# Kernel optimization log

Measured on AMD Instinct MI355X. Metric: run time of the kernel, lower is better.

The kernel has to match this reference:

```python
import jax, jax.numpy as jnp
import numpy as np

IN, HID, LAT, NLAYERS = 512, 256, 128, 2
B, T = 64, 512


def _init_params():
    key = jax.random.key(1)
    ks = jax.random.split(key, 24)

    def g(k, shape):
        fan_in = shape[-1]
        return (jax.random.normal(k, shape, jnp.float32) / np.sqrt(fan_in)).astype(jnp.float32)

    z = lambda n: jnp.zeros((n,), jnp.float32)
    return {
        # input projection
        'Wp': g(ks[0], (HID, IN)), 'bp': z(HID),
        # GRU layer 0 (input = hidden+latent = 384)
        'Wih0': g(ks[1], (3 * HID, HID + LAT)), 'Whh0': g(ks[2], (3 * HID, HID)),
        'bih0': z(3 * HID), 'bhh0': z(3 * HID),
        # GRU layer 1 (input = hidden)
        'Wih1': g(ks[3], (3 * HID, HID)), 'Whh1': g(ks[4], (3 * HID, HID)),
        'bih1': z(3 * HID), 'bhh1': z(3 * HID),
        # prior net
        'Wpr1': g(ks[5], (HID, HID)), 'bpr1': z(HID),
        'Wpr2': g(ks[6], (2 * LAT, HID)), 'bpr2': z(2 * LAT),
        # posterior net
        'Wpo1': g(ks[7], (HID, 2 * HID)), 'bpo1': z(HID),
        'Wpo2': g(ks[8], (2 * LAT, HID)), 'bpo2': z(2 * LAT),
        # decoder
        'Wd1': g(ks[9], (HID, HID + LAT)), 'bd1': z(HID),
        'Wd2': g(ks[10], (2 * IN, HID)), 'bd2': z(2 * IN),
    }


def setup_inputs() -> dict:
    key = jax.random.key(0)
    inp = {
        'x_seq': jax.random.normal(key, (B, T, IN), jnp.float32),
        'hidden': jnp.zeros((NLAYERS, B, HID), jnp.float32),
    }
    inp.update(_init_params())
    return inp


def _gelu(x):
    return jax.nn.gelu(x, approximate=False)  # torch default GELU is exact (erf)


def _gru_cell(x, h, Wih, Whh, bih, bhh):
    gi = x @ Wih.T + bih
    gh = h @ Whh.T + bhh
    ir, iz, inn = jnp.split(gi, 3, axis=-1)
    hr, hz, hn = jnp.split(gh, 3, axis=-1)
    r = jax.nn.sigmoid(ir + hr)
    zg = jax.nn.sigmoid(iz + hz)
    n = jnp.tanh(inn + r * hn)
    return (1.0 - zg) * n + zg * h


def _forward(x_seq, hidden, Wp, bp, Wih0, Whh0, bih0, bhh0, Wih1, Whh1, bih1, bhh1,
             Wpr1, bpr1, Wpr2, bpr2, Wpo1, bpo1, Wpo2, bpo2, Wd1, bd1, Wd2, bd2):
    x_proj = x_seq @ Wp.T + bp          # (B,T,HID)
    xs = jnp.swapaxes(x_proj, 0, 1)     # (T,B,HID)

    def step(h_carry, xt):
        h_prev = h_carry[-1]
        # prior p(z_t | h_{t-1})
        pp = _gelu(h_prev @ Wpr1.T + bpr1) @ Wpr2.T + bpr2
        p_mu, p_lv = jnp.split(pp, 2, axis=-1)
        # posterior q(z_t | h_{t-1}, x_t)
        qp = _gelu(jnp.concatenate([h_prev, xt], -1) @ Wpo1.T + bpo1) @ Wpo2.T + bpo2
        q_mu, q_lv = jnp.split(qp, 2, axis=-1)
        z_t = q_mu  # eval mode: use posterior mean
        # KL(q||p) diagonal Gaussians
        kl = 0.5 * (p_lv - q_lv + (jnp.exp(q_lv) + (q_mu - p_mu) ** 2) / jnp.exp(p_lv) - 1.0)
        kl = kl.sum(-1).mean()
        # 2-layer GRU single step
        gin = jnp.concatenate([xt, z_t], -1)
        h0 = _gru_cell(gin, h_carry[0], Wih0, Whh0, bih0, bhh0)
        h1 = _gru_cell(h0, h_carry[1], Wih1, Whh1, bih1, bhh1)
        h_new = jnp.stack([h0, h1], 0)
        # decode
        op = _gelu(jnp.concatenate([h1, z_t], -1) @ Wd1.T + bd1) @ Wd2.T + bd2
        o_mu, o_lv = jnp.split(op, 2, axis=-1)
        return h_new, (o_mu, o_lv, kl)

    hidden_f, (mus, lvs, kls) = jax.lax.scan(step, hidden, xs)
    pred_mu = jnp.swapaxes(mus, 0, 1)   # (B,T,IN)
    pred_lv = jnp.swapaxes(lvs, 0, 1)
    return pred_mu, pred_lv, kls.mean(), hidden_f


def reference(x_seq, hidden, Wp, bp, Wih0, Whh0, bih0, bhh0, Wih1, Whh1, bih1, bhh1,
              Wpr1, bpr1, Wpr2, bpr2, Wpo1, bpo1, Wpo2, bpo2, Wd1, bd1, Wd2, bd2):
    return _forward(x_seq, hidden, Wp, bp, Wih0, Whh0, bih0, bhh0, Wih1, Whh1, bih1, bhh1,
                    Wpr1, bpr1, Wpr2, bpr2, Wpo1, bpo1, Wpo2, bpo2, Wd1, bd1, Wd2, bd2)
```

## Files before the change

### kernel.cpp

```cpp
#include <hip/hip_runtime.h>
#include <math.h>

#define T_STEPS 512
#define NB      64
#define HID     256
#define IN_DIM  512
#define NWG     16

typedef __attribute__((ext_vector_type(8))) short bh8;
typedef __attribute__((ext_vector_type(4))) float f32x4;

#define SWZ(row, k, Kw) ((row)*(Kw) + ((k) ^ (((row)&7)*8)))

__device__ __forceinline__ float bf2f(unsigned short u) {
  union { unsigned u; float f; } v; v.u = ((unsigned)u) << 16; return v.f;
}
__device__ __forceinline__ unsigned short f2bf(float f) {
  union { float f; unsigned u; } v; v.f = f;
  unsigned r = v.u + 0x7FFFu + ((v.u >> 16) & 1u);
  return (unsigned short)(r >> 16);
}
__device__ __forceinline__ float geluf(float x) {
  return 0.5f * x * (1.f + erff(x * 0.70710678118654752f));
}
__device__ __forceinline__ float sigmf_(float x) { return 1.f / (1.f + __expf(-x)); }

__device__ __forceinline__ f32x4 mfma16(bh8 a, bh8 b, f32x4 c) {
  return __builtin_amdgcn_mfma_f32_16x16x32_bf16(a, b, c, 0, 0, 0);
}

__device__ __forceinline__ bh8 ldsh(const unsigned short* p) {
  bh8 r;
  asm volatile("global_load_dwordx4 %0, %1, off sc0 sc1" : "=v"(r) : "v"(p));
  return r;
}
__device__ __forceinline__ void stsh(unsigned short* p, unsigned short v) {
  unsigned v32 = v;
  asm volatile("global_store_short %0, %1, off sc0 sc1" :: "v"(p), "v"(v32) : "memory");
}
__device__ __forceinline__ void waitv0() {
  asm volatile("s_waitcnt vmcnt(0)" ::: "memory");
  __builtin_amdgcn_sched_barrier(0);
}

struct PrepArgs {
  const float *hidden;
  const float *Wp, *Wpo1, *Whh0, *Whh1, *Wih1, *Wih0, *Wpo2, *Wpr1, *Wpr2, *Wd1, *Wd2;
  unsigned short *Wp_b, *Wpo1cat, *Whh0_b, *Whh1_b, *Wih1_b, *WBcat, *Wpo2_b, *Wpr1_b, *Wpr2_b, *Wd1cat, *Wd2_b;
  unsigned short *H1_0, *h0b;
  unsigned *flags;
};

__global__ void prep1(PrepArgs a) {
  const int task = blockIdx.y;
  const int stride = gridDim.x * blockDim.x;
  const int i0 = blockIdx.x * blockDim.x + threadIdx.x;
  switch (task) {
    case 0:  for (int i=i0;i<131072;i+=stride) a.Wp_b[i]   = f2bf(a.Wp[i]);   break;
    case 1:  for (int i=i0;i<131072;i+=stride) a.Wpo1cat[i]= f2bf(a.Wpo1[i]); break;
    case 2:  for (int i=i0;i<196608;i+=stride) a.Whh0_b[i] = f2bf(a.Whh0[i]); break;
    case 3:  for (int i=i0;i<196608;i+=stride) a.Whh1_b[i] = f2bf(a.Whh1[i]); break;
    case 4:  for (int i=i0;i<196608;i+=stride) a.Wih1_b[i] = f2bf(a.Wih1[i]); break;
    case 5:  for (int i=i0;i<196608;i+=stride) { int c=i>>8, k=i&255;
               a.WBcat[c*512+k] = f2bf(a.Wih0[c*384+k]); } break;
    case 6:  for (int i=i0;i<65536;i+=stride)  a.Wpo2_b[i] = f2bf(a.Wpo2[i]); break;
    case 7:  for (int i=i0;i<65536;i+=stride)  a.Wpr1_b[i] = f2bf(a.Wpr1[i]); break;
    case 8:  for (int i=i0;i<65536;i+=stride)  a.Wpr2_b[i] = f2bf(a.Wpr2[i]); break;
    case 9:  for (int i=i0;i<98304;i+=stride)  a.Wd1cat[i] = f2bf(a.Wd1[i]);  break;
    case 10: for (int i=i0;i<262144;i+=stride) a.Wd2_b[i]  = f2bf(a.Wd2[i]);  break;
    case 11: for (int i=i0;i<16384;i+=stride)  a.H1_0[i] = f2bf(a.hidden[16384+i]); break;
    case 12: for (int i=i0;i<16384;i+=stride)  a.h0b[i]  = f2bf(a.hidden[i]);       break;
    case 15: for (int i=i0;i<1024;i+=stride)   a.flags[i] = 0u;                     break;
    default: break;
  }
}

__global__ void prep2(const float* __restrict__ Wih0, const float* __restrict__ Wpo2,
                      const float* __restrict__ bih0, const float* __restrict__ bpo2,
                      unsigned short* __restrict__ WBcat, float* __restrict__ bk0) {
  const int c = blockIdx.x;
  const int k = threadIdx.x;
  const float* wrow = Wih0 + c*384 + 256;
  float acc = 0.f;
  for (int j = 0; j < 128; ++j) acc += wrow[j] * Wpo2[j*256 + k];
  WBcat[c*512 + 256 + k] = f2bf(acc);
  if (k == 0) {
    float b = bih0[c];
    for (int j = 0; j < 128; ++j) b += wrow[j] * bpo2[j];
    bk0[c] = b;
  }
}

template<int EPI, bool A1F, bool A2F>
__global__ __launch_bounds__(256, 2) void gemm_k(
    const void* __restrict__ A1_, int lda1, int K1,
    const void* __restrict__ A2_, int lda2, int K2,
    const unsigned short* __restrict__ W, const float* __restrict__ bias,
    void* __restrict__ out_, int M, int N)
{
  __shared__ unsigned short sA[64*64];
  __shared__ unsigned short sW[64*64];
  const int m0 = blockIdx.x * 64, n0 = blockIdx.y * 64;
  const int tid = threadIdx.x, lane = tid & 63, wave = tid >> 6;
  const int Ktot = K1 + K2;
  f32x4 zero = {0.f,0.f,0.f,0.f};
  f32x4 acc[4] = {zero, zero, zero, zero};

  for (int kc = 0; kc < Ktot; kc += 64) {
    __syncthreads();
    #pragma unroll
    for (int i = 0; i < 2; ++i) {
      int cidx = tid*2 + i;
      int r = cidx >> 3, ko = (cidx & 7) * 8;
      int kg = kc + ko;
      alignas(16) unsigned short tmp[8];
      if (kg < K1) {
        if (A1F) {
          const float* p = (const float*)A1_ + (size_t)(m0 + r)*lda1 + kg;
          #pragma unroll
          for (int j = 0; j < 8; ++j) tmp[j] = f2bf(p[j]);
        } else {
          const unsigned short* p = (const unsigned short*)A1_ + (size_t)(m0 + r)*lda1 + kg;
          *(bh8*)tmp = *(const bh8*)p;
        }
      } else {
        int k2 = kg - K1;
        if (A2F) {
          const float* p = (const float*)A2_ + (size_t)(m0 + r)*lda2 + k2;
          #pragma unroll
          for (int j = 0; j < 8; ++j) tmp[j] = f2bf(p[j]);
        } else {
          const unsigned short* p = (const unsigned short*)A2_ + (size_t)(m0 + r)*lda2 + k2;
          *(bh8*)tmp = *(const bh8*)p;
        }
      }
      *(bh8*)&sA[SWZ(r, ko, 64)] = *(bh8*)tmp;
    }
    #pragma unroll
    for (int i = 0; i < 2; ++i) {
      int cidx = tid*2 + i;
      int r = cidx >> 3, ko = (cidx & 7) * 8;
      const unsigned short* p = W + (size_t)(n0 + r)*Ktot + kc + ko;
      *(bh8*)&sW[SWZ(r, ko, 64)] = *(const bh8*)p;
    }
    __syncthreads();
    #pragma unroll
    for (int ks = 0; ks < 2; ++ks) {
      int k0 = ks*32 + ((lane >> 4) << 3);
      int ar = 16*wave + (lane & 15);
      bh8 a = *(const bh8*)&sA[SWZ(ar, k0, 64)];
      #pragma unroll
      for (int nt = 0; nt < 4; ++nt) {
        int wr = nt*16 + (lane & 15);
        bh8 b = *(const bh8*)&sW[SWZ(wr, k0, 64)];
        acc[nt] = mfma16(a, b, acc[nt]);
      }
    }
  }
  #pragma unroll
  for (int nt = 0; nt < 4; ++nt) {
    int col = n0 + nt*16 + (lane & 15);
    float bv = bias[col];
    #pragma unroll
    for (int r = 0; r < 4; ++r) {
      int row = m0 + 16*wave + ((lane >> 4) << 2) + r;
      float v = acc[nt][r] + bv;
      if constexpr (EPI == 0) {
        ((float*)out_)[(size_t)row*N + col] = v;
      } else if constexpr (EPI == 1) {
        ((unsigned short*)out_)[(size_t)row*N + col] = f2bf(v);
      } else if constexpr (EPI == 2) {
        int b = row >> 9, t = row & 511;
        ((unsigned short*)out_)[((size_t)t*64 + b)*N + col] = f2bf(v);
      } else if constexpr (EPI == 3) {
        ((unsigned short*)out_)[(size_t)row*N + col] = f2bf(geluf(v));
      } else {
        int t = row >> 6, b = row & 63;
        float* o = (float*)out_;
        if (col < 512) o[(size_t)b*262144 + (size_t)t*512 + col] = v;
        else o[16777216 + (size_t)b*262144 + (size_t)t*512 + (col - 512)] = v;
      }
    }
  }
}

__device__ __forceinline__ void wbar_arrive(unsigned* flags, int g, int w, int lane, unsigned epoch) {
  asm volatile("s_waitcnt vmcnt(0)" ::: "memory");
  if (lane == 0) {
    unsigned* fp = flags + (g*4 + w)*16;
    asm volatile("global_store_dword %0, %1, off sc0 sc1" :: "v"(fp), "v"(epoch) : "memory");
  }
}
__device__ __forceinline__ void wbar_wait(unsigned* flags, int w, int lane, unsigned epoch) {
  if (lane < NWG) {
    const unsigned* fp = flags + (lane*4 + w)*16;
    unsigned v;
    do {
      asm volatile("global_load_dword %0, %1, off sc0 sc1\n\ts_waitcnt vmcnt(0)"
                   : "=v"(v) : "v"(fp) : "memory");
    } while (v < epoch);
  }
  __builtin_amdgcn_sched_barrier(0);
}

#define SEQ_LDS_BYTES ((16*512 + 48*256 + 48*256 + 48*512 + 48*256) * 2)

__global__ __launch_bounds__(256, 1) void seq_kernel(
    const unsigned short* __restrict__ gWQ,
    const unsigned short* __restrict__ gWH0,
    const unsigned short* __restrict__ gWH1,
    const unsigned short* __restrict__ gWB,
    const unsigned short* __restrict__ gWI1,
    const float* __restrict__ bpo1, const float* __restrict__ bhh0,
    const float* __restrict__ bhh1, const float* __restrict__ bih1,
    const float* __restrict__ bk0,
    const float* __restrict__ hidden0,
    const unsigned short* __restrict__ Xp,
    unsigned short* __restrict__ QP1,
    unsigned short* __restrict__ H1,
    unsigned short* __restrict__ h0b,
    unsigned* __restrict__ flags,
    float* __restrict__ outHid)
{
  extern __shared__ unsigned short lds[];
  unsigned short* WQ  = lds;
  unsigned short* WH0 = WQ  + 16*512;
  unsigned short* WH1 = WH0 + 48*256;
  unsigned short* WB  = WH1 + 48*256;
  unsigned short* WI1 = WB  + 48*512;
  const int g = blockIdx.x;
  const int tid = threadIdx.x;
  const int wave = tid >> 6, lane = tid & 63;

  for (int i = tid; i < 16*64; i += 256) { int p = i >> 6, ci = (i & 63) * 8;
    *(bh8*)&WQ[SWZ(p, ci, 512)] = *(const bh8*)&gWQ[(size_t)(16*g + p)*512 + ci]; }
  for (int i = tid; i < 48*32; i += 256) { int p = i >> 5, ci = (i & 31) * 8;
    int c = ((p >> 4) << 8) + 16*g + (p & 15);
    *(bh8*)&WH0[SWZ(p, ci, 256)] = *(const bh8*)&gWH0[(size_t)c*256 + ci]; }
  for (int i = tid; i < 48*32; i += 256) { int p = i >> 5, ci = (i & 31) * 8;
    int c = ((p >> 4) << 8) + 16*g + (p & 15);
    *(bh8*)&WH1[SWZ(p, ci, 256)] = *(const bh8*)&gWH1[(size_t)c*256 + ci]; }
  for (int i = tid; i < 48*64; i += 256) { int p = i >> 6, ci = (i & 63) * 8;
    int c = ((p >> 4) << 8) + 16*g + (p & 15);
    *(bh8*)&WB[SWZ(p, ci, 512)] = *(const bh8*)&gWB[(size_t)c*512 + ci]; }
  for (int i = tid; i < 48*32; i += 256) { int p = i >> 5, ci = (i & 31) * 8;
    int c = ((p >> 4) << 8) + 16*g + (p & 15);
    *(bh8*)&WI1[SWZ(p, ci, 256)] = *(const bh8*)&gWI1[(size_t)c*256 + ci]; }
  __syncthreads();

  const int col   = 16*g + (lane & 15);
  const int arow  = 16*wave + (lane & 15);
  const int crow0 = 16*wave + ((lane >> 4) << 2);
  const int koff  = ((lane >> 4) << 3);
  const float bq = bpo1[col];
  float bh0v[3], bh1v[3], bi1v[3], bk0v[3];
  #pragma unroll
  for (int e = 0; e < 3; ++e) {
    bh0v[e] = bhh0[e*256 + col]; bh1v[e] = bhh1[e*256 + col];
    bi1v[e] = bih1[e*256 + col]; bk0v[e] = bk0[e*256 + col];
  }
  float h0s[4], h1s[4];
  #pragma unroll
  for (int r = 0; r < 4; ++r) {
    h0s[r] = hidden0[(size_t)(crow0 + r)*HID + col];
    h1s[r] = hidden0[16384 + (size_t)(crow0 + r)*HID + col];
  }
  const f32x4 zero = {0.f,0.f,0.f,0.f};
  unsigned epoch = 0;

  f32x4 gh0a[3] = {zero, zero, zero};
  {
    bh8 h0i[8];
    #pragma unroll
    for (int j = 0; j < 8; ++j) h0i[j] = ldsh(h0b + (size_t)arow*HID + j*32 + koff);
    waitv0();
    #pragma unroll
    for (int ks = 0; ks < 8; ++ks) {
      int k0 = ks*32 + koff;
      #pragma unroll
      for (int e = 0; e < 3; ++e)
        gh0a[e] = mfma16(h0i[ks], *(const bh8*)&WH0[SWZ(e*16 + (lane&15), k0, 256)], gh0a[e]);
    }
  }
  bh8 xpr[8];
  #pragma unroll
  for (int j = 0; j < 8; ++j) xpr[j] = *(const bh8*)(Xp + (size_t)arow*HID + j*32 + koff);

  #pragma unroll 1
  for (int t = 0; t < T_STEPS; ++t) {
    const unsigned short* h1b = H1 + (size_t)t * (NB*HID);
    unsigned short* qp1t = QP1 + (size_t)t * (NB*HID);

    bh8 h1r[8];
    #pragma unroll
    for (int j = 0; j < 8; ++j) h1r[j] = ldsh(h1b + (size_t)arow*HID + j*32 + koff);
    waitv0();
    f32x4 aQ0 = zero, aQ1 = zero;
    #pragma unroll
    for (int ks = 0; ks < 8; ++ks) {
      int k0 = ks*32 + koff;
      aQ0 = mfma16(h1r[ks], *(const bh8*)&WQ[SWZ(lane & 15, k0, 512)], aQ0);
      aQ1 = mfma16(xpr[ks], *(const bh8*)&WQ[SWZ(lane & 15, 256 + k0, 512)], aQ1);
    }
    f32x4 gh1a[3] = {zero, zero, zero};
    #pragma unroll
    for (int ks = 0; ks < 8; ++ks) {
      int k0 = ks*32 + koff;
      #pragma unroll
      for (int e = 0; e < 3; ++e)
        gh1a[e] = mfma16(h1r[ks], *(const bh8*)&WH1[SWZ(e*16 + (lane&15), k0, 256)], gh1a[e]);
    }
    #pragma unroll
    for (int r = 0; r < 4; ++r) {
      float v = geluf(aQ0[r] + aQ1[r] + bq);
      stsh(qp1t + (size_t)(crow0 + r)*HID + col, f2bf(v));
    }
    ++epoch;
    wbar_arrive(flags, g, wave, lane, epoch);
    f32x4 gi[3] = {zero, zero, zero};
    #pragma unroll
    for (int ks = 0; ks < 8; ++ks) {
      int k0 = ks*32 + koff;
      #pragma unroll
      for (int e = 0; e < 3; ++e)
        gi[e] = mfma16(xpr[ks], *(const bh8*)&WB[SWZ(e*16 + (lane&15), k0, 512)], gi[e]);
    }
    wbar_wait(flags, wave, lane, epoch);

    bh8 qpr[8];
    #pragma unroll
    for (int j = 0; j < 8; ++j) qpr[j] = ldsh(qp1t + (size_t)arow*HID + j*32 + koff);
    waitv0();
    #pragma unroll
    for (int ks = 0; ks < 8; ++ks) {
      int k0 = ks*32 + koff;
      #pragma unroll
      for (int e = 0; e < 3; ++e)
        gi[e] = mfma16(qpr[ks], *(const bh8*)&WB[SWZ(e*16 + (lane&15), 256 + k0, 512)], gi[e]);
    }
    #pragma unroll
    for (int r = 0; r < 4; ++r) {
      float rr = sigmf_(gi[0][r] + bk0v[0] + gh0a[0][r] + bh0v[0]);
      float zz = sigmf_(gi[1][r] + bk0v[1] + gh0a[1][r] + bh0v[1]);
      float nn = tanhf(gi[2][r] + bk0v[2] + rr*(gh0a[2][r] + bh0v[2]));
      float hn = (1.f - zz)*nn + zz*h0s[r];
      h0s[r] = hn;
      stsh(h0b + (size_t)(crow0 + r)*HID + col, f2bf(hn));
    }
    ++epoch;
    wbar_arrive(flags, g, wave, lane, epoch);
    if (t + 1 < T_STEPS) {
      const unsigned short* xq = Xp + (size_t)(t + 1) * (NB*HID);
      #pragma unroll
      for (int j = 0; j < 8; ++j) xpr[j] = *(const bh8*)(xq + (size_t)arow*HID + j*32 + koff);
    }
    wbar_wait(flags, wave, lane, epoch);

    bh8 h0n[8];
    #pragma unroll
    for (int j = 0; j < 8; ++j) h0n[j] = ldsh(h0b + (size_t)arow*HID + j*32 + koff);
    waitv0();
    f32x4 gi1[3] = {zero, zero, zero};
    #pragma unroll
    for (int ks = 0; ks < 8; ++ks) {
      int k0 = ks*32 + koff;
      #pragma unroll
      for (int e = 0; e < 3; ++e)
        gi1[e] = mfma16(h0n[ks], *(const bh8*)&WI1[SWZ(e*16 + (lane&15), k0, 256)], gi1[e]);
    }
    unsigned short* h1n = H1 + (size_t)(t + 1) * (NB*HID);
    #pragma unroll
    for (int r = 0; r < 4; ++r) {
      float rr = sigmf_(gi1[0][r] + bi1v[0] + gh1a[0][r] + bh1v[0]);
      float zz = sigmf_(gi1[1][r] + bi1v[1] + gh1a[1][r] + bh1v[1]);
      float nn = tanhf(gi1[2][r] + bi1v[2] + rr*(gh1a[2][r] + bh1v[2]));
      float hv = (1.f - zz)*nn + zz*h1s[r];
      h1s[r] = hv;
      stsh(h1n + (size_t)(crow0 + r)*HID + col, f2bf(hv));
    }
    ++epoch;
    wbar_arrive(flags, g, wave, lane, epoch);
    if (t + 1 < T_STEPS) {
      gh0a[0] = zero; gh0a[1] = zero; gh0a[2] = zero;
      #pragma unroll
      for (int ks = 0; ks < 8; ++ks) {
        int k0 = ks*32 + koff;
        #pragma unroll
        for (int e = 0; e < 3; ++e)
          gh0a[e] = mfma16(h0n[ks], *(const bh8*)&WH0[SWZ(e*16 + (lane&15), k0, 256)], gh0a[e]);
      }
    }
    wbar_wait(flags, wave, lane, epoch);
  }

  #pragma unroll
  for (int r = 0; r < 4; ++r) {
    int row = crow0 + r;
    outHid[(size_t)row*HID + col]         = h0s[r];
    outHid[16384 + (size_t)row*HID + col] = h1s[r];
  }
}

__global__ void kl1(const float* __restrict__ Q, const unsigned short* __restrict__ Ppb,
                    float* __restrict__ part) {
  const int m0 = blockIdx.x * 64;
  float s = 0.f;
  for (int i = threadIdx.x; i < 64*128; i += 256) {
    int m = m0 + (i >> 7), j = i & 127;
    float qm = Q[(size_t)m*256 + j],        ql = Q[(size_t)m*256 + 128 + j];
    float pm = bf2f(Ppb[(size_t)m*256 + j]), pl = bf2f(Ppb[(size_t)m*256 + 128 + j]);
    float d = qm - pm;
    s += 0.5f * (pl - ql + (expf(ql) + d*d) * expf(-pl) - 1.f);
  }
  for (int o = 32; o > 0; o >>= 1) s += __shfl_down(s, o);
  __shared__ float red[4];
  if ((threadIdx.x & 63) == 0) red[threadIdx.x >> 6] = s;
  __syncthreads();
  if (threadIdx.x == 0) part[blockIdx.x] = red[0] + red[1] + red[2] + red[3];
}
__global__ void kl2(const float* __restrict__ part, float* __restrict__ out) {
  float s = 0.f;
  for (int i = threadIdx.x; i < 512; i += 256) s += part[i];
  for (int o = 32; o > 0; o >>= 1) s += __shfl_down(s, o);
  __shared__ float red[4];
  if ((threadIdx.x & 63) == 0) red[threadIdx.x >> 6] = s;
  __syncthreads();
  if (threadIdx.x == 0) out[0] = (red[0] + red[1] + red[2] + red[3]) / 32768.f;
}

extern "C" void kernel_launch(void* const* d_in, const int* in_sizes, int n_in,
                              void* d_out, int out_size, void* d_ws, size_t ws_size,
                              hipStream_t stream) {
  const float* x_seq  = (const float*)d_in[0];
  const float* hidden = (const float*)d_in[1];
  const float* Wp   = (const float*)d_in[2];  const float* bp   = (const float*)d_in[3];
  const float* Wih0 = (const float*)d_in[4];  const float* Whh0 = (const float*)d_in[5];
  const float* bih0 = (const float*)d_in[6];  const float* bhh0 = (const float*)d_in[7];
  const float* Wih1 = (const float*)d_in[8];  const float* Whh1 = (const float*)d_in[9];
  const float* bih1 = (const float*)d_in[10]; const float* bhh1 = (const float*)d_in[11];
  const float* Wpr1 = (const float*)d_in[12]; const float* bpr1 = (const float*)d_in[13];
  const float* Wpr2 = (const float*)d_in[14]; const float* bpr2 = (const float*)d_in[15];
  const float* Wpo1 = (const float*)d_in[16]; const float* bpo1 = (const float*)d_in[17];
  const float* Wpo2 = (const float*)d_in[18]; const float* bpo2 = (const float*)d_in[19];
  const float* Wd1  = (const float*)d_in[20]; const float* bd1  = (const float*)d_in[21];
  const float* Wd2  = (const float*)d_in[22]; const float* bd2  = (const float*)d_in[23];

  char* ws = (char*)d_ws;
  char* Ob = (char*)d_out;
  float* O = (float*)d_out;

  unsigned short* Xp  = (unsigned short*)(Ob + 0);
  unsigned short* QP1 = (unsigned short*)(Ob + (16u << 20));
  unsigned short* H1  = (unsigned short*)(Ob + (32u << 20));
  float*          Q   = (float*)         (Ob + (64u << 20));
  unsigned short* P1b = (unsigned short*)(Ob + (96u << 20));
  unsigned short* Ppb = (unsigned short*)(Ob + (112u << 20));

  unsigned short* D1b     = (unsigned short*)(ws + 0);
  char* wb = ws + 16777216;
  unsigned short* Wp_b    = (unsigned short*)(wb + 0);
  unsigned short* Wpo1cat = (unsigned short*)(wb + 262144);
  unsigned short* Whh0_b  = (unsigned short*)(wb + 524288);
  unsigned short* Whh1_b  = (unsigned short*)(wb + 917504);
  unsigned short* Wih1_b  = (unsigned short*)(wb + 1310720);
  unsigned short* WBcat   = (unsigned short*)(wb + 1703936);
  unsigned short* Wpo2_b  = (unsigned short*)(wb + 2490368);
  unsigned short* Wpr1_b  = (unsigned short*)(wb + 2621440);
  unsigned short* Wpr2_b  = (unsigned short*)(wb + 2752512);
  unsigned short* Wd1cat  = (unsigned short*)(wb + 2883584);
  unsigned short* Wd2_b   = (unsigned short*)(wb + 3080192);
  float*    bk0    = (float*)(ws + 20381696);
  unsigned short* h0b = (unsigned short*)(ws + 20515840);
  unsigned* flags  = (unsigned*)(ws + 20548608);
  float*    klpart = (float*)(ws + 20552704);

  PrepArgs pa;
  pa.hidden = hidden;
  pa.Wp = Wp; pa.Wpo1 = Wpo1; pa.Whh0 = Whh0; pa.Whh1 = Whh1; pa.Wih1 = Wih1;
  pa.Wih0 = Wih0; pa.Wpo2 = Wpo2; pa.Wpr1 = Wpr1; pa.Wpr2 = Wpr2; pa.Wd1 = Wd1; pa.Wd2 = Wd2;
  pa.Wp_b = Wp_b; pa.Wpo1cat = Wpo1cat; pa.Whh0_b = Whh0_b; pa.Whh1_b = Whh1_b;
  pa.Wih1_b = Wih1_b; pa.WBcat = WBcat; pa.Wpo2_b = Wpo2_b; pa.Wpr1_b = Wpr1_b;
  pa.Wpr2_b = Wpr2_b; pa.Wd1cat = Wd1cat; pa.Wd2_b = Wd2_b;
  pa.H1_0 = H1; pa.h0b = h0b; pa.flags = flags;
  prep1<<<dim3(64, 16), 256, 0, stream>>>(pa);
  prep2<<<768, 256, 0, stream>>>(Wih0, Wpo2, bih0, bpo2, WBcat, bk0);

  gemm_k<2, true, false><<<dim3(512, 4), 256, 0, stream>>>(
      x_seq, 512, 512, nullptr, 0, 0, Wp_b, bp, Xp, 32768, 256);

  (void)hipFuncSetAttribute((const void*)seq_kernel,
                            hipFuncAttributeMaxDynamicSharedMemorySize, SEQ_LDS_BYTES);
  seq_kernel<<<NWG, 256, SEQ_LDS_BYTES, stream>>>(
      Wpo1cat, Whh0_b, Whh1_b, WBcat, Wih1_b,
      bpo1, bhh0, bhh1, bih1, bk0, hidden,
      Xp, QP1, H1, h0b, flags, O + 33554433);

  gemm_k<0, false, false><<<dim3(512, 4), 256, 0, stream>>>(
      QP1, 256, 256, nullptr, 0, 0, Wpo2_b, bpo2, Q, 32768, 256);
  gemm_k<3, false, false><<<dim3(512, 4), 256, 0, stream>>>(
      H1, 256, 256, nullptr, 0, 0, Wpr1_b, bpr1, P1b, 32768, 256);
  gemm_k<1, false, false><<<dim3(512, 4), 256, 0, stream>>>(
      P1b, 256, 256, nullptr, 0, 0, Wpr2_b, bpr2, Ppb, 32768, 256);
  kl1<<<512, 256, 0, stream>>>(Q, Ppb, klpart);
  kl2<<<1, 256, 0, stream>>>(klpart, O + 33554432);
  gemm_k<3, false, true><<<dim3(512, 4), 256, 0, stream>>>(
      H1 + 16384, 256, 256, Q, 256, 128, Wd1cat, bd1, D1b, 32768, 256);
  gemm_k<4, false, false><<<dim3(512, 16), 256, 0, stream>>>(
      D1b, 256, 256, nullptr, 0, 0, Wd2_b, bd2, (void*)O, 32768, 1024);

  (void)in_sizes; (void)n_in; (void)out_size; (void)ws_size;
}
```

Baseline: 5.313 ms.

## Replace per-workgroup flag barrier with atomic counter barrier and reschedule step MFMAs

The grid barrier changes from each workgroup writing its own epoch flag, with up to 16 lanes polling them, to a per-wave atomic counter that lane 0 polls against epoch*16. The x-dependent part of the prior/posterior projection (aQ1p) is now computed one step ahead, overlapped with the gh0 MFMAs. The GELU store is moved earlier, and the gi MFMAs are interleaved with gh1 before the first barrier. The goal is to cut barrier polling traffic and shorten the serial critical path per timestep. The trade-off is that the third arrive now waits until after the gh0 and aQ1p MFMAs, and all workgroups contend on one atomic counter.

```diff
diff --git a/kernel.cpp b/kernel.cpp
--- a/kernel.cpp
+++ b/kernel.cpp
@@ -184,21 +184,19 @@
   }
 }
 
-__device__ __forceinline__ void wbar_arrive(unsigned* flags, int g, int w, int lane, unsigned epoch) {
+__device__ __forceinline__ void pbar_arrive(unsigned* cnt, int w, int lane) {
   asm volatile("s_waitcnt vmcnt(0)" ::: "memory");
+  if (lane == 0)
+    (void)__hip_atomic_fetch_add(cnt + w*32, 1u, __ATOMIC_RELAXED, __HIP_MEMORY_SCOPE_AGENT);
+}
+__device__ __forceinline__ void pbar_wait(unsigned* cnt, int w, int lane, unsigned target) {
   if (lane == 0) {
-    unsigned* fp = flags + (g*4 + w)*16;
-    asm volatile("global_store_dword %0, %1, off sc0 sc1" :: "v"(fp), "v"(epoch) : "memory");
-  }
-}
-__device__ __forceinline__ void wbar_wait(unsigned* flags, int w, int lane, unsigned epoch) {
-  if (lane < NWG) {
-    const unsigned* fp = flags + (lane*4 + w)*16;
+    const unsigned* cp = cnt + w*32;
     unsigned v;
     do {
       asm volatile("global_load_dword %0, %1, off sc0 sc1\n\ts_waitcnt vmcnt(0)"
-                   : "=v"(v) : "v"(fp) : "memory");
-    } while (v < epoch);
+                   : "=v"(v) : "v"(cp) : "memory");
+    } while (v < target);
   }
   __builtin_amdgcn_sched_barrier(0);
 }
@@ -285,6 +283,12 @@
   bh8 xpr[8];
   #pragma unroll
   for (int j = 0; j < 8; ++j) xpr[j] = *(const bh8*)(Xp + (size_t)arow*HID + j*32 + koff);
+  f32x4 aQ1p = zero;
+  #pragma unroll
+  for (int ks = 0; ks < 8; ++ks) {
+    int k0 = ks*32 + koff;
+    aQ1p = mfma16(xpr[ks], *(const bh8*)&WQ[SWZ(lane & 15, 256 + k0, 512)], aQ1p);
+  }
 
   #pragma unroll 1
   for (int t = 0; t < T_STEPS; ++t) {
@@ -295,37 +299,31 @@
     #pragma unroll
     for (int j = 0; j < 8; ++j) h1r[j] = ldsh(h1b + (size_t)arow*HID + j*32 + koff);
     waitv0();
-    f32x4 aQ0 = zero, aQ1 = zero;
+    f32x4 aQ0 = zero;
     #pragma unroll
     for (int ks = 0; ks < 8; ++ks) {
       int k0 = ks*32 + koff;
       aQ0 = mfma16(h1r[ks], *(const bh8*)&WQ[SWZ(lane & 15, k0, 512)], aQ0);
-      aQ1 = mfma16(xpr[ks], *(const bh8*)&WQ[SWZ(lane & 15, 256 + k0, 512)], aQ1);
+    }
+    #pragma unroll
+    for (int r = 0; r < 4; ++r) {
+      float v = geluf(aQ0[r] + aQ1p[r] + bq);
+      stsh(qp1t + (size_t)(crow0 + r)*HID + col, f2bf(v));
     }
     f32x4 gh1a[3] = {zero, zero, zero};
+    f32x4 gi[3]   = {zero, zero, zero};
     #pragma unroll
     for (int ks = 0; ks < 8; ++ks) {
       int k0 = ks*32 + koff;
       #pragma unroll
-      for (int e = 0; e < 3; ++e)
+      for (int e = 0; e < 3; ++e) {
         gh1a[e] = mfma16(h1r[ks], *(const bh8*)&WH1[SWZ(e*16 + (lane&15), k0, 256)], gh1a[e]);
-    }
-    #pragma unroll
-    for (int r = 0; r < 4; ++r) {
-      float v = geluf(aQ0[r] + aQ1[r] + bq);
-      stsh(qp1t + (size_t)(crow0 + r)*HID + col, f2bf(v));
+        gi[e]   = mfma16(xpr[ks], *(const bh8*)&WB[SWZ(e*16 + (lane&15), k0, 512)], gi[e]);
+      }
     }
     ++epoch;
-    wbar_arrive(flags, g, wave, lane, epoch);
-    f32x4 gi[3] = {zero, zero, zero};
-    #pragma unroll
-    for (int ks = 0; ks < 8; ++ks) {
-      int k0 = ks*32 + koff;
-      #pragma unroll
-      for (int e = 0; e < 3; ++e)
-        gi[e] = mfma16(xpr[ks], *(const bh8*)&WB[SWZ(e*16 + (lane&15), k0, 512)], gi[e]);
-    }
-    wbar_wait(flags, wave, lane, epoch);
+    pbar_arrive(flags, wave, lane);
+    pbar_wait(flags, wave, lane, epoch * 16u);
 
     bh8 qpr[8];
     #pragma unroll
@@ -348,13 +346,13 @@
       stsh(h0b + (size_t)(crow0 + r)*HID + col, f2bf(hn));
     }
     ++epoch;
-    wbar_arrive(flags, g, wave, lane, epoch);
+    pbar_arrive(flags, wave, lane);
     if (t + 1 < T_STEPS) {
       const unsigned short* xq = Xp + (size_t)(t + 1) * (NB*HID);
       #pragma unroll
       for (int j = 0; j < 8; ++j) xpr[j] = *(const bh8*)(xq + (size_t)arow*HID + j*32 + koff);
     }
-    wbar_wait(flags, wave, lane, epoch);
+    pbar_wait(flags, wave, lane, epoch * 16u);
 
     bh8 h0n[8];
     #pragma unroll
@@ -378,19 +376,21 @@
       h1s[r] = hv;
       stsh(h1n + (size_t)(crow0 + r)*HID + col, f2bf(hv));
     }
-    ++epoch;
-    wbar_arrive(flags, g, wave, lane, epoch);
     if (t + 1 < T_STEPS) {
       gh0a[0] = zero; gh0a[1] = zero; gh0a[2] = zero;
+      aQ1p = zero;
       #pragma unroll
       for (int ks = 0; ks < 8; ++ks) {
         int k0 = ks*32 + koff;
         #pragma unroll
         for (int e = 0; e < 3; ++e)
           gh0a[e] = mfma16(h0n[ks], *(const bh8*)&WH0[SWZ(e*16 + (lane&15), k0, 256)], gh0a[e]);
+        aQ1p = mfma16(xpr[ks], *(const bh8*)&WQ[SWZ(lane & 15, 256 + k0, 512)], aQ1p);
       }
     }
-    wbar_wait(flags, wave, lane, epoch);
+    ++epoch;
+    pbar_arrive(flags, wave, lane);
+    pbar_wait(flags, wave, lane, epoch * 16u);
   }
 
   #pragma unroll
```

Result: slower. 6.255 ms (+17.7%).

## Block the exchanged hidden-state layout and move independent MFMAs off the critical path

Applied to the files above, without the earlier changes.

Shared per-step buffers (h0, H1, QP1) now use a column-blocked layout, so each workgroup's 16-column slice is one contiguous 2 KB block and its bf16 stores coalesce. The downstream GEMMs gain a reader for that layout. Inside the recurrent loop, the x-dependent posterior term (aQ1) is computed for the next step during the previous step's tail. The x-part of the layer-0 input gates is moved ahead of the barrier arrive, and the flag stride is widened to reduce false sharing between flags. The aim is to shorten the serial work between cross-workgroup barriers, at the cost of more registers and a more complex layout contract between kernels.

```diff
diff --git a/kernel.cpp b/kernel.cpp
--- a/kernel.cpp
+++ b/kernel.cpp
@@ -11,6 +11,8 @@
 typedef __attribute__((ext_vector_type(4))) float f32x4;
 
 #define SWZ(row, k, Kw) ((row)*(Kw) + ((k) ^ (((row)&7)*8)))
+
+#define BADDR(row, col) ((((col) >> 4) << 10) + ((row) << 4) + ((col) & 15))
 
 __device__ __forceinline__ float bf2f(unsigned short u) {
   union { unsigned u; float f; } v; v.u = ((unsigned)u) << 16; return v.f;
@@ -68,9 +70,11 @@
     case 8:  for (int i=i0;i<65536;i+=stride)  a.Wpr2_b[i] = f2bf(a.Wpr2[i]); break;
     case 9:  for (int i=i0;i<98304;i+=stride)  a.Wd1cat[i] = f2bf(a.Wd1[i]);  break;
     case 10: for (int i=i0;i<262144;i+=stride) a.Wd2_b[i]  = f2bf(a.Wd2[i]);  break;
-    case 11: for (int i=i0;i<16384;i+=stride)  a.H1_0[i] = f2bf(a.hidden[16384+i]); break;
-    case 12: for (int i=i0;i<16384;i+=stride)  a.h0b[i]  = f2bf(a.hidden[i]);       break;
-    case 15: for (int i=i0;i<1024;i+=stride)   a.flags[i] = 0u;                     break;
+    case 11: for (int i=i0;i<16384;i+=stride) { int r=i>>8, c=i&255;
+               a.H1_0[BADDR(r,c)] = f2bf(a.hidden[16384+i]); } break;
+    case 12: for (int i=i0;i<16384;i+=stride) { int r=i>>8, c=i&255;
+               a.h0b[BADDR(r,c)]  = f2bf(a.hidden[i]); } break;
+    case 15: for (int i=i0;i<2048;i+=stride)   a.flags[i] = 0u;  break;
     default: break;
   }
 }
@@ -91,7 +95,24 @@
   }
 }
 
-template<int EPI, bool A1F, bool A2F>
+template<int FMT>
+__device__ __forceinline__ void ldA(const void* A, int lda, int row, int k,
+                                    unsigned short* tmp) {
+  if constexpr (FMT == 1) {
+    const float* p = (const float*)A + (size_t)row*lda + k;
+    #pragma unroll
+    for (int j = 0; j < 8; ++j) tmp[j] = f2bf(p[j]);
+  } else if constexpr (FMT == 3) {
+    const unsigned short* p = (const unsigned short*)A
+        + ((size_t)(row >> 6))*16384 + (size_t)(k >> 4)*1024
+        + (size_t)(row & 63)*16 + (k & 15);
+    *(bh8*)tmp = *(const bh8*)p;
+  } else {
+    *(bh8*)tmp = *(const bh8*)((const unsigned short*)A + (size_t)row*lda + k);
+  }
+}
+
+template<int EPI, int A1T, int A2T>
 __global__ __launch_bounds__(256, 2) void gemm_k(
     const void* __restrict__ A1_, int lda1, int K1,
     const void* __restrict__ A2_, int lda2, int K2,
@@ -114,26 +135,8 @@
       int r = cidx >> 3, ko = (cidx & 7) * 8;
       int kg = kc + ko;
       alignas(16) unsigned short tmp[8];
-      if (kg < K1) {
-        if (A1F) {
-          const float* p = (const float*)A1_ + (size_t)(m0 + r)*lda1 + kg;
-          #pragma unroll
-          for (int j = 0; j < 8; ++j) tmp[j] = f2bf(p[j]);
-        } else {
-          const unsigned short* p = (const unsigned short*)A1_ + (size_t)(m0 + r)*lda1 + kg;
-          *(bh8*)tmp = *(const bh8*)p;
-        }
-      } else {
-        int k2 = kg - K1;
-        if (A2F) {
-          const float* p = (const float*)A2_ + (size_t)(m0 + r)*lda2 + k2;
-          #pragma unroll
-          for (int j = 0; j < 8; ++j) tmp[j] = f2bf(p[j]);
-        } else {
-          const unsigned short* p = (const unsigned short*)A2_ + (size_t)(m0 + r)*lda2 + k2;
-          *(bh8*)tmp = *(const bh8*)p;
-        }
-      }
+      if (kg < K1) ldA<A1T>(A1_, lda1, m0 + r, kg, tmp);
+      else         ldA<A2T>(A2_, lda2, m0 + r, kg - K1, tmp);
       *(bh8*)&sA[SWZ(r, ko, 64)] = *(bh8*)tmp;
     }
     #pragma unroll
@@ -187,13 +190,13 @@
 __device__ __forceinline__ void wbar_arrive(unsigned* flags, int g, int w, int lane, unsigned epoch) {
   asm volatile("s_waitcnt vmcnt(0)" ::: "memory");
   if (lane == 0) {
-    unsigned* fp = flags + (g*4 + w)*16;
+    unsigned* fp = flags + (g*4 + w)*32;
     asm volatile("global_store_dword %0, %1, off sc0 sc1" :: "v"(fp), "v"(epoch) : "memory");
   }
 }
 __device__ __forceinline__ void wbar_wait(unsigned* flags, int w, int lane, unsigned epoch) {
   if (lane < NWG) {
-    const unsigned* fp = flags + (lane*4 + w)*16;
+    const unsigned* fp = flags + (lane*4 + w)*32;
     unsigned v;
     do {
       asm volatile("global_load_dword %0, %1, off sc0 sc1\n\ts_waitcnt vmcnt(0)"
@@ -252,6 +255,7 @@
   const int arow  = 16*wave + (lane & 15);
   const int crow0 = 16*wave + ((lane >> 4) << 2);
   const int koff  = ((lane >> 4) << 3);
+  const int l15   = lane & 15;
   const float bq = bpo1[col];
   float bh0v[3], bh1v[3], bi1v[3], bk0v[3];
   #pragma unroll
@@ -266,77 +270,78 @@
     h1s[r] = hidden0[16384 + (size_t)(crow0 + r)*HID + col];
   }
   const f32x4 zero = {0.f,0.f,0.f,0.f};
+  const int pst = (g << 10) + l15;
   unsigned epoch = 0;
 
   f32x4 gh0a[3] = {zero, zero, zero};
   {
     bh8 h0i[8];
     #pragma unroll
-    for (int j = 0; j < 8; ++j) h0i[j] = ldsh(h0b + (size_t)arow*HID + j*32 + koff);
+    for (int j = 0; j < 8; ++j) h0i[j] = ldsh(h0b + BADDR(arow, j*32 + koff));
     waitv0();
     #pragma unroll
     for (int ks = 0; ks < 8; ++ks) {
       int k0 = ks*32 + koff;
       #pragma unroll
       for (int e = 0; e < 3; ++e)
-        gh0a[e] = mfma16(h0i[ks], *(const bh8*)&WH0[SWZ(e*16 + (lane&15), k0, 256)], gh0a[e]);
+        gh0a[e] = mfma16(h0i[ks], *(const bh8*)&WH0[SWZ(e*16 + l15, k0, 256)], gh0a[e]);
     }
   }
   bh8 xpr[8];
   #pragma unroll
   for (int j = 0; j < 8; ++j) xpr[j] = *(const bh8*)(Xp + (size_t)arow*HID + j*32 + koff);
+  f32x4 aQ1p = zero;
+  #pragma unroll
+  for (int ks = 0; ks < 8; ++ks) {
+    int k0 = ks*32 + koff;
+    aQ1p = mfma16(xpr[ks], *(const bh8*)&WQ[SWZ(l15, 256 + k0, 512)], aQ1p);
+  }
 
   #pragma unroll 1
   for (int t = 0; t < T_STEPS; ++t) {
-    const unsigned short* h1b = H1 + (size_t)t * (NB*HID);
-    unsigned short* qp1t = QP1 + (size_t)t * (NB*HID);
+    const unsigned short* h1slot = H1 + (size_t)t * (NB*HID);
+    unsigned short* qpslot = QP1 + (size_t)t * (NB*HID);
 
     bh8 h1r[8];
     #pragma unroll
-    for (int j = 0; j < 8; ++j) h1r[j] = ldsh(h1b + (size_t)arow*HID + j*32 + koff);
+    for (int j = 0; j < 8; ++j) h1r[j] = ldsh(h1slot + BADDR(arow, j*32 + koff));
     waitv0();
-    f32x4 aQ0 = zero, aQ1 = zero;
+    f32x4 aQ0 = zero;
     #pragma unroll
     for (int ks = 0; ks < 8; ++ks) {
       int k0 = ks*32 + koff;
-      aQ0 = mfma16(h1r[ks], *(const bh8*)&WQ[SWZ(lane & 15, k0, 512)], aQ0);
-      aQ1 = mfma16(xpr[ks], *(const bh8*)&WQ[SWZ(lane & 15, 256 + k0, 512)], aQ1);
+      aQ0 = mfma16(h1r[ks], *(const bh8*)&WQ[SWZ(l15, k0, 512)], aQ0);
+    }
+    #pragma unroll
+    for (int r = 0; r < 4; ++r) {
+      float v = geluf(aQ0[r] + aQ1p[r] + bq);
+      stsh(qpslot + pst + ((crow0 + r) << 4), f2bf(v));
     }
     f32x4 gh1a[3] = {zero, zero, zero};
+    f32x4 gi[3]   = {zero, zero, zero};
     #pragma unroll
     for (int ks = 0; ks < 8; ++ks) {
       int k0 = ks*32 + koff;
       #pragma unroll
-      for (int e = 0; e < 3; ++e)
-        gh1a[e] = mfma16(h1r[ks], *(const bh8*)&WH1[SWZ(e*16 + (lane&15), k0, 256)], gh1a[e]);
-    }
-    #pragma unroll
-    for (int r = 0; r < 4; ++r) {
-      float v = geluf(aQ0[r] + aQ1[r] + bq);
-      stsh(qp1t + (size_t)(crow0 + r)*HID + col, f2bf(v));
+      for (int e = 0; e < 3; ++e) {
+        gh1a[e] = mfma16(h1r[ks], *(const bh8*)&WH1[SWZ(e*16 + l15, k0, 256)], gh1a[e]);
+        gi[e]   = mfma16(xpr[ks], *(const bh8*)&WB[SWZ(e*16 + l15, k0, 512)], gi[e]);
+      }
     }
     ++epoch;
     wbar_arrive(flags, g, wave, lane, epoch);
-    f32x4 gi[3] = {zero, zero, zero};
+    wbar_wait(flags, wave, lane, epoch);
+
+    bh8 qpr[8];
+    #pragma unroll
+    for (int j = 0; j < 8; ++j) qpr[j] = ldsh(qpslot + BADDR(arow, j*32 + koff));
+    waitv0();
     #pragma unroll
     for (int ks = 0; ks < 8; ++ks) {
       int k0 = ks*32 + koff;
       #pragma unroll
       for (int e = 0; e < 3; ++e)
-        gi[e] = mfma16(xpr[ks], *(const bh8*)&WB[SWZ(e*16 + (lane&15), k0, 512)], gi[e]);
-    }
-    wbar_wait(flags, wave, lane, epoch);
-
-    bh8 qpr[8];
-    #pragma unroll
-    for (int j = 0; j < 8; ++j) qpr[j] = ldsh(qp1t + (size_t)arow*HID + j*32 + koff);
-    waitv0();
-    #pragma unroll
-    for (int ks = 0; ks < 8; ++ks) {
-      int k0 = ks*32 + koff;
-      #pragma unroll
-      for (int e = 0; e < 3; ++e)
-        gi[e] = mfma16(qpr[ks], *(const bh8*)&WB[SWZ(e*16 + (lane&15), 256 + k0, 512)], gi[e]);
+        gi[e] = mfma16(qpr[ks], *(const bh8*)&WB[SWZ(e*16 + l15, 256 + k0, 512)], gi[e]);
     }
     #pragma unroll
     for (int r = 0; r < 4; ++r) {
@@ -345,7 +350,7 @@
       float nn = tanhf(gi[2][r] + bk0v[2] + rr*(gh0a[2][r] + bh0v[2]));
       float hn = (1.f - zz)*nn + zz*h0s[r];
       h0s[r] = hn;
-      stsh(h0b + (size_t)(crow0 + r)*HID + col, f2bf(hn));
+      stsh(h0b + pst + ((crow0 + r) << 4), f2bf(hn));
     }
     ++epoch;
     wbar_arrive(flags, g, wave, lane, epoch);
@@ -358,7 +363,7 @@
 
     bh8 h0n[8];
     #pragma unroll
-    for (int j = 0; j < 8; ++j) h0n[j] = ldsh(h0b + (size_t)arow*HID + j*32 + koff);
+    for (int j = 0; j < 8; ++j) h0n[j] = ldsh(h0b + BADDR(arow, j*32 + koff));
     waitv0();
     f32x4 gi1[3] = {zero, zero, zero};
     #pragma unroll
@@ -366,9 +371,9 @@
       int k0 = ks*32 + koff;
       #pragma unroll
       for (int e = 0; e < 3; ++e)
-        gi1[e] = mfma16(h0n[ks], *(const bh8*)&WI1[SWZ(e*16 + (lane&15), k0, 256)], gi1[e]);
-    }
-    unsigned short* h1n = H1 + (size_t)(t + 1) * (NB*HID);
+        gi1[e] = mfma16(h0n[ks], *(const bh8*)&WI1[SWZ(e*16 + l15, k0, 256)], gi1[e]);
+    }
+    unsigned short* h1next = H1 + (size_t)(t + 1) * (NB*HID);
     #pragma unroll
     for (int r = 0; r < 4; ++r) {
       float rr = sigmf_(gi1[0][r] + bi1v[0] + gh1a[0][r] + bh1v[0]);
@@ -376,18 +381,20 @@
       float nn = tanhf(gi1[2][r] + bi1v[2] + rr*(gh1a[2][r] + bh1v[2]));
       float hv = (1.f - zz)*nn + zz*h1s[r];
       h1s[r] = hv;
-      stsh(h1n + (size_t)(crow0 + r)*HID + col, f2bf(hv));
+      stsh(h1next + pst + ((crow0 + r) << 4), f2bf(hv));
     }
     ++epoch;
     wbar_arrive(flags, g, wave, lane, epoch);
     if (t + 1 < T_STEPS) {
       gh0a[0] = zero; gh0a[1] = zero; gh0a[2] = zero;
+      aQ1p = zero;
       #pragma unroll
       for (int ks = 0; ks < 8; ++ks) {
         int k0 = ks*32 + koff;
         #pragma unroll
         for (int e = 0; e < 3; ++e)
-          gh0a[e] = mfma16(h0n[ks], *(const bh8*)&WH0[SWZ(e*16 + (lane&15), k0, 256)], gh0a[e]);
+          gh0a[e] = mfma16(h0n[ks], *(const bh8*)&WH0[SWZ(e*16 + l15, k0, 256)], gh0a[e]);
+        aQ1p = mfma16(xpr[ks], *(const bh8*)&WQ[SWZ(l15, 256 + k0, 512)], aQ1p);
       }
     }
     wbar_wait(flags, wave, lane, epoch);
@@ -472,7 +479,7 @@
   float*    bk0    = (float*)(ws + 20381696);
   unsigned short* h0b = (unsigned short*)(ws + 20515840);
   unsigned* flags  = (unsigned*)(ws + 20548608);
-  float*    klpart = (float*)(ws + 20552704);
+  float*    klpart = (float*)(ws + 20557056);
 
   PrepArgs pa;
   pa.hidden = hidden;
@@ -485,7 +492,7 @@
   prep1<<<dim3(64, 16), 256, 0, stream>>>(pa);
   prep2<<<768, 256, 0, stream>>>(Wih0, Wpo2, bih0, bpo2, WBcat, bk0);
 
-  gemm_k<2, true, false><<<dim3(512, 4), 256, 0, stream>>>(
+  gemm_k<2, 1, 0><<<dim3(512, 4), 256, 0, stream>>>(
       x_seq, 512, 512, nullptr, 0, 0, Wp_b, bp, Xp, 32768, 256);
 
   (void)hipFuncSetAttribute((const void*)seq_kernel,
@@ -495,17 +502,17 @@
       bpo1, bhh0, bhh1, bih1, bk0, hidden,
       Xp, QP1, H1, h0b, flags, O + 33554433);
 
-  gemm_k<0, false, false><<<dim3(512, 4), 256, 0, stream>>>(
-      QP1, 256, 256, nullptr, 0, 0, Wpo2_b, bpo2, Q, 32768, 256);
-  gemm_k<3, false, false><<<dim3(512, 4), 256, 0, stream>>>(
-      H1, 256, 256, nullptr, 0, 0, Wpr1_b, bpr1, P1b, 32768, 256);
-  gemm_k<1, false, false><<<dim3(512, 4), 256, 0, stream>>>(
+  gemm_k<0, 3, 0><<<dim3(512, 4), 256, 0, stream>>>(
+      QP1, 0, 256, nullptr, 0, 0, Wpo2_b, bpo2, Q, 32768, 256);
+  gemm_k<3, 3, 0><<<dim3(512, 4), 256, 0, stream>>>(
+      H1, 0, 256, nullptr, 0, 0, Wpr1_b, bpr1, P1b, 32768, 256);
+  gemm_k<1, 0, 0><<<dim3(512, 4), 256, 0, stream>>>(
       P1b, 256, 256, nullptr, 0, 0, Wpr2_b, bpr2, Ppb, 32768, 256);
   kl1<<<512, 256, 0, stream>>>(Q, Ppb, klpart);
   kl2<<<1, 256, 0, stream>>>(klpart, O + 33554432);
-  gemm_k<3, false, true><<<dim3(512, 4), 256, 0, stream>>>(
-      H1 + 16384, 256, 256, Q, 256, 128, Wd1cat, bd1, D1b, 32768, 256);
-  gemm_k<4, false, false><<<dim3(512, 16), 256, 0, stream>>>(
+  gemm_k<3, 3, 1><<<dim3(512, 4), 256, 0, stream>>>(
+      H1 + 16384, 0, 256, Q, 256, 128, Wd1cat, bd1, D1b, 32768, 256);
+  gemm_k<4, 0, 0><<<dim3(512, 16), 256, 0, stream>>>(
       D1b, 256, 256, nullptr, 0, 0, Wd2_b, bd2, (void*)O, 32768, 1024);
 
   (void)in_sizes; (void)n_in; (void)out_size; (void)ws_size;
```

Measured after the change: 4.768 ms. 1.11x faster.
